# Kernel tuning notes

Hardware: AMD Instinct MI355X
Metric: run time of the kernel (lower is better)

Reference implementation:

```python
import jax, jax.numpy as jnp
import numpy as np

N_NODES = 50000
N_EDGES = 800000
IN_DIM = 128
ATT_DIM = 128
NEG_SLOPE = 0.01  # nn.LeakyReLU default


def setup_inputs() -> dict:
    key = jax.random.key(0)
    ks = jax.random.split(key, 8)
    x = jax.random.normal(ks[0], (N_NODES, IN_DIM), dtype=jnp.float32)
    src_idx = jax.random.randint(ks[1], (N_EDGES,), 0, N_NODES, dtype=jnp.int32)
    dst_idx = jax.random.randint(ks[2], (N_EDGES,), 0, N_NODES, dtype=jnp.int32)
    # small init scale keeps exp(score) numerically tame
    src_w = jax.random.normal(ks[3], (IN_DIM, ATT_DIM), dtype=jnp.float32) * 0.05
    src_b = jnp.zeros((ATT_DIM,), dtype=jnp.float32)
    dst_w = jax.random.normal(ks[4], (IN_DIM, ATT_DIM), dtype=jnp.float32) * 0.05
    dst_b = jnp.zeros((ATT_DIM,), dtype=jnp.float32)
    att_w = jax.random.normal(ks[5], (ATT_DIM, 1), dtype=jnp.float32) * 0.05
    att_b = jnp.zeros((1,), dtype=jnp.float32)
    return {"x": x, "src_idx": src_idx, "dst_idx": dst_idx,
            "src_w": src_w, "src_b": src_b, "dst_w": dst_w, "dst_b": dst_b,
            "att_w": att_w, "att_b": att_b}


def reference(x, src_idx, dst_idx, src_w, src_b, dst_w, dst_b, att_w, att_b):
    n = x.shape[0]
    # 1) mean aggregation of source features onto destinations (copy_u + mean)
    deg = jax.ops.segment_sum(jnp.ones_like(dst_idx, dtype=x.dtype), dst_idx, num_segments=n)
    h_mean = jax.ops.segment_sum(x[src_idx], dst_idx, num_segments=n)
    h_mean = h_mean / jnp.maximum(deg, 1.0)[:, None]
    # 2) attention projections on nodes (dense GEMMs)
    ha_src = x @ src_w + src_b          # [N, att_dim]
    ha_dst = h_mean @ dst_w + dst_b     # [N, att_dim]
    # 3) per-edge u_add_v -> LeakyReLU -> att Linear -> exp
    e = jax.nn.leaky_relu(ha_src[src_idx] + ha_dst[dst_idx], NEG_SLOPE)  # [E, att_dim]
    s = jnp.exp(e @ att_w + att_b)      # [E, 1]
    # 4) edge softmax: normalize by segment sum over destination
    denom = jax.ops.segment_sum(s, dst_idx, num_segments=n)  # [N, 1]
    a = s / denom[dst_idx]              # [E, 1]
    # 5) u_mul_e weighted aggregation (sum)
    out = jax.ops.segment_sum(x[src_idx] * a, dst_idx, num_segments=n)  # [N, in_dim]
    return out
```

## Files before the change

kernel.cpp:

```cpp
#include <hip/hip_runtime.h>
#include <math.h>

#define N_NODES 50000
#define N_EDGES 800000
#define DIM 128
#define NEG_SLOPE 0.01f
#define CAP 64

#define GEMM_BLOCKS ((N_NODES + 63) / 64)
#define EPB 1024

typedef short v8s __attribute__((ext_vector_type(8)));
typedef float v4f __attribute__((ext_vector_type(4)));

__device__ inline unsigned f2bf2(float a, float b) {
    unsigned ua = __float_as_uint(a);
    unsigned ub = __float_as_uint(b);
    ua = (ua + 0x7fffu + ((ua >> 16) & 1u)) >> 16;
    ub = (ub + 0x7fffu + ((ub >> 16) & 1u)) & 0xffff0000u;
    return ua | ub;
}
__device__ inline float2 bf2f(unsigned u) {
    float2 r;
    r.x = __uint_as_float(u << 16);
    r.y = __uint_as_float(u & 0xffff0000u);
    return r;
}

__device__ inline float2 pka(float2 a, float2 b) {
    return make_float2(a.x + b.x, a.y + b.y);
}
__device__ inline float2 pkfma(float2 a, float2 b, float2 c) {
    return make_float2(fmaf(a.x, b.x, c.x), fmaf(a.y, b.y, c.y));
}
__device__ inline float2 leaky2(float2 v) {
    return make_float2(fmaxf(v.x, v.x * NEG_SLOPE), fmaxf(v.y, v.y * NEG_SLOPE));
}

#define ROR_ADD(v, CTRL) \
    ((v) + __int_as_float(__builtin_amdgcn_update_dpp( \
        0, __float_as_int(v), (CTRL), 0xf, 0xf, false)))

__global__ __launch_bounds__(256) void k_prepw(
    const float* __restrict__ src_w, const float* __restrict__ dst_w,
    unsigned* __restrict__ whT, int* __restrict__ deg)
{
    int gid = blockIdx.x * 256 + threadIdx.x;
    if (gid < 256 * 64) {
        int n = gid >> 6;
        int kk = gid & 63;
        const float* W = (n < 128) ? src_w : dst_w;
        int col = n & 127;
        float w0 = W[(2 * kk) * DIM + col];
        float w1 = W[(2 * kk + 1) * DIM + col];
        whT[gid] = f2bf2(w0, w1);
    }
    if (gid < N_NODES) deg[gid] = 0;
}

__global__ __launch_bounds__(256) void k_scatgemm(
    const int* __restrict__ src, const int* __restrict__ dst,
    int* __restrict__ deg, int* __restrict__ slots,
    const float* __restrict__ x, const unsigned* __restrict__ whT,
    const float* __restrict__ src_b, unsigned* __restrict__ hx_u,
    unsigned* __restrict__ yu)
{
    __shared__ unsigned lds[64][196];
    int bx = blockIdx.x;
    int tid = threadIdx.x;

    int e0 = bx * EPB + tid;
    int sv[4], dv[4];
    #pragma unroll
    for (int i = 0; i < 4; ++i) {
        int e = e0 + i * 256;
        bool v = (e < N_EDGES);
        sv[i] = v ? src[e] : 0;
        dv[i] = v ? dst[e] : 0;
    }

    int wave = tid >> 6;
    int lane = tid & 63;
    int quad = lane >> 4;
    int m = lane & 15;
    int arow = bx * 64 + wave * 16 + m;
    int lr = wave * 16 + m;
    bool live = (arow < N_NODES);

    v8s b[4];
    #pragma unroll
    for (int k0 = 0; k0 < 4; ++k0) {
        float4 f0 = make_float4(0.f, 0.f, 0.f, 0.f);
        float4 f1 = f0;
        if (live) {
            const float4* xp = (const float4*)(x + (size_t)arow * DIM + k0 * 32 + quad * 8);
            f0 = xp[0];
            f1 = xp[1];
        }
        union { unsigned u[4]; v8s s; } pk;
        pk.u[0] = f2bf2(f0.x, f0.y);
        pk.u[1] = f2bf2(f0.z, f0.w);
        pk.u[2] = f2bf2(f1.x, f1.y);
        pk.u[3] = f2bf2(f1.z, f1.w);
        b[k0] = pk.s;
        int c = k0 * 32 + quad * 8 + 1;
        lds[lr][c + 0] = pk.u[0];
        lds[lr][c + 2] = pk.u[1];
        lds[lr][c + 4] = pk.u[2];
        lds[lr][c + 6] = pk.u[3];
    }

    #pragma unroll
    for (int i = 0; i < 4; ++i) {
        int e = e0 + i * 256;
        if (e < N_EDGES) {
            int pos = atomicAdd(&deg[dv[i]], 1);
            if (pos < CAP) slots[dv[i] * CAP + pos] = sv[i] * 64;
        }
    }

    #pragma unroll
    for (int nt = 0; nt < 16; ++nt) {
        v4f acc = {0.f, 0.f, 0.f, 0.f};
        const uint4* ap = (const uint4*)(whT + (size_t)(nt * 16 + m) * 64 + quad * 4);
        #pragma unroll
        for (int k0 = 0; k0 < 4; ++k0) {
            union { uint4 u; v8s s; } af;
            af.u = ap[k0 * 4];
            acc = __builtin_amdgcn_mfma_f32_16x16x32_bf16(af.s, b[k0], acc, 0, 0, 0);
        }
        if (nt < 8) {
            float4 bia = ((const float4*)src_b)[nt * 4 + quad];
            int c = nt * 16 + quad * 4;
            lds[lr][c]     = f2bf2(acc[0] + bia.x, acc[1] + bia.y);
            lds[lr][c + 2] = f2bf2(acc[2] + bia.z, acc[3] + bia.w);
        } else {
            int c = 64 + nt * 8 + quad * 2;
            lds[lr][c]     = f2bf2(acc[0], acc[1]);
            lds[lr][c + 1] = f2bf2(acc[2], acc[3]);
        }
    }
    __syncthreads();

    int rbase = bx * 64;
    for (int i = tid; i < 64 * 32; i += 256) {
        int r = i >> 5, c = i & 31;
        int row = rbase + r;
        if (row < N_NODES)
            ((uint4*)(hx_u + (size_t)row * 128))[c] = *(const uint4*)&lds[r][c * 4];
    }
    for (int i = tid; i < 64 * 16; i += 256) {
        int r = i >> 4, c = i & 15;
        int row = rbase + r;
        if (row < N_NODES)
            ((uint4*)(yu + (size_t)row * 64))[c] = *(const uint4*)&lds[r][128 + c * 4];
    }
}

__global__ __launch_bounds__(256) void k_fuse(
    const uint2* __restrict__ hx, const unsigned* __restrict__ yu,
    const int* __restrict__ slots, const int* __restrict__ deg,
    const float* __restrict__ dst_b, const float* __restrict__ att_w,
    const float* __restrict__ att_b, float* __restrict__ out)
{
    int g = blockIdx.x * 256 + threadIdx.x;
    int node = g >> 6;
    int lane = g & 63;
    int grp = lane >> 4;
    int sl = lane & 15;
    int cnt = deg[node];
    if (cnt == 0) {
        if (grp < 2) {
            v4f z = {0.f, 0.f, 0.f, 0.f};
            __builtin_nontemporal_store(z, (v4f*)out + node * 32 + 2 * sl + grp);
        }
        return;
    }
    int cc = (cnt < CAP) ? cnt : CAP;
    int trips = (cc + 3) >> 2;
    int myoff = (lane < cc) ? slots[node * CAP + lane] : 0;

    float2 hd01 = {0.f, 0.f}, hd23 = {0.f, 0.f};
    float2 hd45 = {0.f, 0.f}, hd67 = {0.f, 0.f};
    #pragma unroll 2
    for (int t = 0; t < trips; ++t) {
        int i = 4 * t + grp;
        bool valid = (i < cc);
        int off = __shfl(myoff, valid ? i : 0);
        if (valid) {
            uint4 q = *((const uint4*)(yu + off) + sl);
            hd01 = pka(hd01, bf2f(q.x));
            hd23 = pka(hd23, bf2f(q.y));
            hd45 = pka(hd45, bf2f(q.z));
            hd67 = pka(hd67, bf2f(q.w));
        }
    }
    float inv = 1.0f / (float)cnt;
    float4 db0 = ((const float4*)dst_b)[2 * sl];
    float4 db1 = ((const float4*)dst_b)[2 * sl + 1];
    #define XRED(f) { f += __shfl_xor(f, 32); f += __shfl_xor(f, 16); f *= inv; }
    XRED(hd01.x) XRED(hd01.y) XRED(hd23.x) XRED(hd23.y)
    XRED(hd45.x) XRED(hd45.y) XRED(hd67.x) XRED(hd67.y)
    #undef XRED
    hd01.x += db0.x; hd01.y += db0.y; hd23.x += db0.z; hd23.y += db0.w;
    hd45.x += db1.x; hd45.y += db1.y; hd67.x += db1.z; hd67.y += db1.w;

    float4 aw0 = ((const float4*)att_w)[2 * sl];
    float4 aw1 = ((const float4*)att_w)[2 * sl + 1];
    float2 aw01 = make_float2(aw0.x, aw0.y), aw23 = make_float2(aw0.z, aw0.w);
    float2 aw45 = make_float2(aw1.x, aw1.y), aw67 = make_float2(aw1.z, aw1.w);
    float ab = att_b[0];
    float2 o01 = {0.f, 0.f}, o23 = {0.f, 0.f};
    float2 o45 = {0.f, 0.f}, o67 = {0.f, 0.f};
    float dsum = 0.f;
    #pragma unroll 2
    for (int t = 0; t < trips; ++t) {
        int i = 4 * t + grp;
        bool valid = (i < cc);
        int off = __shfl(myoff, valid ? i : 0);
        if (valid) {
            const uint4* hp = (const uint4*)(hx + off);
            uint4 qa = hp[2 * sl];
            uint4 qb = hp[2 * sl + 1];
            float2 p2 = {0.f, 0.f};
            p2 = pkfma(leaky2(pka(bf2f(qa.x), hd01)), aw01, p2);
            p2 = pkfma(leaky2(pka(bf2f(qa.z), hd23)), aw23, p2);
            p2 = pkfma(leaky2(pka(bf2f(qb.x), hd45)), aw45, p2);
            p2 = pkfma(leaky2(pka(bf2f(qb.z), hd67)), aw67, p2);
            float p = p2.x + p2.y;
            p = ROR_ADD(p, 0x128);
            p = ROR_ADD(p, 0x124);
            p = ROR_ADD(p, 0x122);
            p = ROR_ADD(p, 0x121);
            float s = __expf(p + ab);
            float2 s2 = make_float2(s, s);
            o01 = pkfma(bf2f(qa.y), s2, o01);
            o23 = pkfma(bf2f(qa.w), s2, o23);
            o45 = pkfma(bf2f(qb.y), s2, o45);
            o67 = pkfma(bf2f(qb.w), s2, o67);
            dsum += s;
        }
    }
    dsum += __shfl_xor(dsum, 32);
    dsum += __shfl_xor(dsum, 16);
    #define XRED2(f) { f += __shfl_xor(f, 32); f += __shfl_xor(f, 16); }
    XRED2(o01.x) XRED2(o01.y) XRED2(o23.x) XRED2(o23.y)
    XRED2(o45.x) XRED2(o45.y) XRED2(o67.x) XRED2(o67.y)
    #undef XRED2
    float r = 1.0f / dsum;
    if (grp < 2) {
        v4f ov;
        if (grp == 0) {
            ov[0] = o01.x * r; ov[1] = o01.y * r; ov[2] = o23.x * r; ov[3] = o23.y * r;
        } else {
            ov[0] = o45.x * r; ov[1] = o45.y * r; ov[2] = o67.x * r; ov[3] = o67.y * r;
        }
        __builtin_nontemporal_store(ov, (v4f*)out + node * 32 + 2 * sl + grp);
    }
}

extern "C" void kernel_launch(void* const* d_in, const int* in_sizes, int n_in,
                              void* d_out, int out_size, void* d_ws, size_t ws_size,
                              hipStream_t stream)
{
    const float* x     = (const float*)d_in[0];
    const int*   src   = (const int*)d_in[1];
    const int*   dst   = (const int*)d_in[2];
    const float* src_w = (const float*)d_in[3];
    const float* src_b = (const float*)d_in[4];
    const float* dst_w = (const float*)d_in[5];
    const float* dst_b = (const float*)d_in[6];
    const float* att_w = (const float*)d_in[7];
    const float* att_b = (const float*)d_in[8];
    float* out = (float*)d_out;
    (void)in_sizes; (void)n_in; (void)out_size; (void)ws_size;

    const size_t NF = (size_t)N_NODES * DIM;

    int* ws = (int*)d_ws;
    int* ideg  = ws;
    int* slots = ws + 50048;
    unsigned* whT = (unsigned*)(ws + 3250048);
    unsigned* yu  = whT + 16384;
    uint2*    hx  = (uint2*)(yu + NF / 2);

    k_prepw<<<256, 256, 0, stream>>>(src_w, dst_w, whT, ideg);

    k_scatgemm<<<GEMM_BLOCKS, 256, 0, stream>>>(
        src, dst, ideg, slots, x, whT, src_b, (unsigned*)hx, yu);

    k_fuse<<<N_NODES * 64 / 256, 256, 0, stream>>>(
        hx, yu, slots, ideg, dst_b, att_w, att_b, out);
}
```

Measured before the change: 253.2 us.

## Use per-wave LDS tiles, drop block barrier, issue degree atomics early

The scatter+GEMM kernel's shared tile is split into per-wave 16-row slices, so each wave stages and writes out its own rows without a block-wide __syncthreads. This cuts LDS per block (64x196 to 4x16x132 words), which may allow more resident blocks. The second GEMM's accumulators stay in registers and reuse the same LDS slice after the first output is written. Degree atomics are issued right after the index loads so their latency overlaps the x loads and MFMA work. The cost is extra register pressure from the eight held accumulators and the per-edge slot positions.

```diff
diff --git a/kernel.cpp b/kernel.cpp
--- a/kernel.cpp
+++ b/kernel.cpp
@@ -65,12 +65,12 @@
     const float* __restrict__ src_b, unsigned* __restrict__ hx_u,
     unsigned* __restrict__ yu)
 {
-    __shared__ unsigned lds[64][196];
+    __shared__ unsigned lds[4][16][132];
+    int tid = threadIdx.x;
     int bx = blockIdx.x;
-    int tid = threadIdx.x;
 
     int e0 = bx * EPB + tid;
-    int sv[4], dv[4];
+    int sv[4], dv[4], pos[4];
     #pragma unroll
     for (int i = 0; i < 4; ++i) {
         int e = e0 + i * 256;
@@ -78,13 +78,19 @@
         sv[i] = v ? src[e] : 0;
         dv[i] = v ? dst[e] : 0;
     }
+    #pragma unroll
+    for (int i = 0; i < 4; ++i) {
+        int e = e0 + i * 256;
+        pos[i] = (e < N_EDGES) ? atomicAdd(&deg[dv[i]], 1) : CAP;
+    }
 
     int wave = tid >> 6;
     int lane = tid & 63;
     int quad = lane >> 4;
     int m = lane & 15;
-    int arow = bx * 64 + wave * 16 + m;
-    int lr = wave * 16 + m;
+    unsigned (*L)[132] = lds[wave];
+    int rbase0 = bx * 64 + wave * 16;
+    int arow = rbase0 + m;
     bool live = (arow < N_NODES);
 
     v8s b[4];
@@ -104,21 +110,17 @@
         pk.u[3] = f2bf2(f1.z, f1.w);
         b[k0] = pk.s;
         int c = k0 * 32 + quad * 8 + 1;
-        lds[lr][c + 0] = pk.u[0];
-        lds[lr][c + 2] = pk.u[1];
-        lds[lr][c + 4] = pk.u[2];
-        lds[lr][c + 6] = pk.u[3];
-    }
-
-    #pragma unroll
-    for (int i = 0; i < 4; ++i) {
-        int e = e0 + i * 256;
-        if (e < N_EDGES) {
-            int pos = atomicAdd(&deg[dv[i]], 1);
-            if (pos < CAP) slots[dv[i] * CAP + pos] = sv[i] * 64;
-        }
-    }
-
+        L[m][c + 0] = pk.u[0];
+        L[m][c + 2] = pk.u[1];
+        L[m][c + 4] = pk.u[2];
+        L[m][c + 6] = pk.u[3];
+    }
+
+    #pragma unroll
+    for (int i = 0; i < 4; ++i)
+        if (pos[i] < CAP) slots[dv[i] * CAP + pos[i]] = sv[i] * 64;
+
+    v4f yacc[8];
     #pragma unroll
     for (int nt = 0; nt < 16; ++nt) {
         v4f acc = {0.f, 0.f, 0.f, 0.f};
@@ -132,28 +134,31 @@
         if (nt < 8) {
             float4 bia = ((const float4*)src_b)[nt * 4 + quad];
             int c = nt * 16 + quad * 4;
-            lds[lr][c]     = f2bf2(acc[0] + bia.x, acc[1] + bia.y);
-            lds[lr][c + 2] = f2bf2(acc[2] + bia.z, acc[3] + bia.w);
+            L[m][c]     = f2bf2(acc[0] + bia.x, acc[1] + bia.y);
+            L[m][c + 2] = f2bf2(acc[2] + bia.z, acc[3] + bia.w);
         } else {
-            int c = 64 + nt * 8 + quad * 2;
-            lds[lr][c]     = f2bf2(acc[0], acc[1]);
-            lds[lr][c + 1] = f2bf2(acc[2], acc[3]);
-        }
-    }
-    __syncthreads();
-
-    int rbase = bx * 64;
-    for (int i = tid; i < 64 * 32; i += 256) {
+            yacc[nt - 8] = acc;
+        }
+    }
+
+    for (int i = lane; i < 512; i += 64) {
         int r = i >> 5, c = i & 31;
-        int row = rbase + r;
+        int row = rbase0 + r;
         if (row < N_NODES)
-            ((uint4*)(hx_u + (size_t)row * 128))[c] = *(const uint4*)&lds[r][c * 4];
-    }
-    for (int i = tid; i < 64 * 16; i += 256) {
+            ((uint4*)(hx_u + (size_t)row * 128))[c] = *(const uint4*)&L[r][c * 4];
+    }
+
+    #pragma unroll
+    for (int t = 0; t < 8; ++t) {
+        int c = t * 8 + quad * 2;
+        L[m][c]     = f2bf2(yacc[t][0], yacc[t][1]);
+        L[m][c + 1] = f2bf2(yacc[t][2], yacc[t][3]);
+    }
+    for (int i = lane; i < 256; i += 64) {
         int r = i >> 4, c = i & 15;
-        int row = rbase + r;
+        int row = rbase0 + r;
         if (row < N_NODES)
-            ((uint4*)(yu + (size_t)row * 64))[c] = *(const uint4*)&lds[r][128 + c * 4];
+            ((uint4*)(yu + (size_t)row * 64))[c] = *(const uint4*)&L[r][c * 4];
     }
 }
 
```

After: 248.6 us. About the same (-1.8%).
